# Kernel optimization log

Measured on AMD Instinct MI355X. Metric: run time of the kernel, lower is better.

The kernel has to match this reference:

```python
import jax, jax.numpy as jnp
import numpy as np

N, E, G = 50000, 800000, 64   # nodes, edges, graphs
F, H, O = 6, 256, 2           # in_dim, hidden_dim, out_dim
NE, K, L = 8, 2, 4            # n_experts, top_k, n_layers


def setup_inputs() -> dict:
    key = jax.random.key(0)
    ks = jax.random.split(key, 12)
    s = 0.05
    return {
        "x": jax.random.normal(ks[0], (N, F), jnp.float32),
        "edge_index": jax.random.randint(ks[1], (2, E), 0, N),
        "batch": jnp.sort(jax.random.randint(ks[2], (N,), 0, G)),
        "enc_W": jax.random.normal(ks[3], (F, H), jnp.float32) * s,
        "enc_b": jnp.zeros((H,), jnp.float32),
        "rtr_W1": jax.random.normal(ks[4], (H + 2, H), jnp.float32) * s,
        "rtr_b1": jnp.zeros((H,), jnp.float32),
        "rtr_W2": jax.random.normal(ks[5], (H, NE), jnp.float32) * s,
        "rtr_b2": jnp.zeros((NE,), jnp.float32),
        "hid_Wr": jax.random.normal(ks[6], (L - 1, NE, H, H), jnp.float32) * s,
        "hid_Wn": jax.random.normal(ks[7], (L - 1, NE, H, H), jnp.float32) * s,
        "hid_b": jnp.zeros((L - 1, NE, H), jnp.float32),
        "out_Wr": jax.random.normal(ks[8], (NE, H, O), jnp.float32) * s,
        "out_Wn": jax.random.normal(ks[9], (NE, H, O), jnp.float32) * s,
        "out_b": jnp.zeros((NE, O), jnp.float32),
    }


def reference(x, edge_index, batch, enc_W, enc_b, rtr_W1, rtr_b1, rtr_W2, rtr_b2,
              hid_Wr, hid_Wn, hid_b, out_Wr, out_Wn, out_b):
    src, dst = edge_index[0], edge_index[1]

    # SharedBusEncoder: Linear + ReLU
    h = jax.nn.relu(x @ enc_W + enc_b)  # [N, H]

    # graph_size_features: per-graph node/edge counts, log-scaled, per node
    ones_n = jnp.ones((N,), h.dtype)
    nodes_per_g = jax.ops.segment_sum(ones_n, batch, num_segments=G)
    edges_per_g = jax.ops.segment_sum(jnp.ones((E,), h.dtype), batch[src], num_segments=G)
    size_feat = jnp.stack([jnp.log(nodes_per_g + 1.0)[batch],
                           jnp.log(edges_per_g + 1.0)[batch]], axis=-1)  # [N, 2]

    # BaseRouter: 2-layer MLP -> logits [N, NE]
    r = jax.nn.relu(jnp.concatenate([h, size_feat], axis=-1) @ rtr_W1 + rtr_b1)
    logits = r @ rtr_W2 + rtr_b2

    # sparse_routing (eval mode): softmax over top-k logits, scattered to dense mask
    vals, idx = jax.lax.top_k(logits, K)  # [N, K]
    w = jax.nn.softmax(vals, axis=-1)
    sparse = jnp.zeros((N, NE), h.dtype).at[jnp.arange(N)[:, None], idx].set(w)

    # Dense all-expert GraphConv stacks, mask-sum combine
    def graph_conv(he, Wr, Wn, b):
        agg = jax.ops.segment_sum(he[src], dst, num_segments=N)  # sum-aggregate neighbors
        return he @ Wr + agg @ Wn + b

    out = jnp.zeros((N, O), h.dtype)
    for e in range(NE):
        he = h
        for l in range(L - 1):
            he = jax.nn.relu(graph_conv(he, hid_Wr[l, e], hid_Wn[l, e], hid_b[l, e]))
        ye = graph_conv(he, out_Wr[e], out_Wn[e], out_b[e])  # [N, O]
        out = out + ye * sparse[:, e:e + 1]
    return out
```

## Files before the change

### kernel.cpp

```cpp
#include <hip/hip_runtime.h>
#include <cstdint>

#define NN 50000
#define EE 800000
#define GG 64

typedef unsigned short u16;
typedef __attribute__((ext_vector_type(8))) short bf16x8;
typedef __attribute__((ext_vector_type(4))) float f32x4;

__device__ __forceinline__ float bf2f(u16 v) { return __uint_as_float(((unsigned)v) << 16); }
__device__ __forceinline__ u16 f2bf(float f) {
  unsigned u = __float_as_uint(f);
  return (u16)((u + 0x7fffu + ((u >> 16) & 1u)) >> 16);
}

__device__ __forceinline__ void gload_lds16(const void* g, void* l) {
  __builtin_amdgcn_global_load_lds(
      (const __attribute__((address_space(1))) void*)g,
      (__attribute__((address_space(3))) void*)l,
      16, 0, 0);
}

__global__ void k_sentinel(float* out) { out[threadIdx.x] = 1e12f; }

__global__ __launch_bounds__(256) void k_hist(const int* __restrict__ ei,
                                              int* __restrict__ deg,
                                              int* __restrict__ outdeg) {
  int i = blockIdx.x * 256 + threadIdx.x;
  if (i < EE) {
    atomicAdd(&outdeg[ei[i]], 1);
    atomicAdd(&deg[ei[EE + i]], 1);
  }
}

__global__ __launch_bounds__(256) void k_graph_feats(const int* __restrict__ batch,
                                                     const int* __restrict__ outdeg,
                                                     float* __restrict__ gf) {
  __shared__ int red[256];
  int g = blockIdx.x, tid = threadIdx.x;
  auto lb = [&](int v) {
    int lo = 0, hi = NN;
    while (lo < hi) { int m = (lo + hi) >> 1; if (batch[m] < v) lo = m + 1; else hi = m; }
    return lo;
  };
  int bs = lb(g), be = lb(g + 1);
  int s = 0;
  for (int i = bs + tid; i < be; i += 256) s += outdeg[i];
  red[tid] = s;
  __syncthreads();
  for (int off = 128; off > 0; off >>= 1) {
    if (tid < off) red[tid] += red[tid + off];
    __syncthreads();
  }
  if (tid == 0) {
    gf[g * 2] = logf((float)(be - bs) + 1.f);
    gf[g * 2 + 1] = logf((float)red[0] + 1.f);
  }
}

__global__ __launch_bounds__(256) void k_router(
    const float* __restrict__ x, const float* __restrict__ encW, const float* __restrict__ encb,
    const int* __restrict__ batch, const float* __restrict__ gf,
    const float* __restrict__ W1, const float* __restrict__ b1,
    const float* __restrict__ W2, const float* __restrict__ b2,
    float* __restrict__ sparse, u16* __restrict__ hb_out) {
  __shared__ __align__(16) float hs_t[258][8];
  __shared__ __align__(16) float rs_t[256][8];
  __shared__ float part2[4][64];
  __shared__ float xv[8][6];
  __shared__ float sf[8][2];
  __shared__ float lg[8][8];
  int tid = threadIdx.x;
  int nb = blockIdx.x * 8;
  if (tid < 48) {
    int r = tid / 6, k = tid % 6;
    xv[r][k] = x[(nb + r) * 6 + k];
  }
  if (tid >= 48 && tid < 56) {
    int r = tid - 48;
    int g = batch[nb + r];
    sf[r][0] = gf[g * 2];
    sf[r][1] = gf[g * 2 + 1];
  }
  __syncthreads();
  {
    float wcol[6];
#pragma unroll
    for (int k = 0; k < 6; ++k) wcol[k] = encW[k * 256 + tid];
    float bb = encb[tid];
#pragma unroll
    for (int r = 0; r < 8; ++r) {
      float s = bb;
#pragma unroll
      for (int k = 0; k < 6; ++k) s += xv[r][k] * wcol[k];
      float h = fmaxf(s, 0.f);
      hs_t[tid][r] = h;
      hb_out[(nb + r) * 256 + tid] = f2bf(h);
    }
  }
  if (tid < 16) {
    int r = tid >> 1, c = tid & 1;
    hs_t[256 + c][r] = sf[r][c];
  }
  __syncthreads();
  float acc[8];
  {
    float bb = b1[tid];
#pragma unroll
    for (int r = 0; r < 8; ++r) acc[r] = bb;
  }
  int k = 0;
#pragma unroll 4
  for (; k < 256; ++k) {
    float w = W1[k * 256 + tid];
    float4 ha = *(const float4*)&hs_t[k][0];
    float4 hb4 = *(const float4*)&hs_t[k][4];
    acc[0] += ha.x * w; acc[1] += ha.y * w; acc[2] += ha.z * w; acc[3] += ha.w * w;
    acc[4] += hb4.x * w; acc[5] += hb4.y * w; acc[6] += hb4.z * w; acc[7] += hb4.w * w;
  }
  for (; k < 258; ++k) {
    float w = W1[k * 256 + tid];
    float4 ha = *(const float4*)&hs_t[k][0];
    float4 hb4 = *(const float4*)&hs_t[k][4];
    acc[0] += ha.x * w; acc[1] += ha.y * w; acc[2] += ha.z * w; acc[3] += ha.w * w;
    acc[4] += hb4.x * w; acc[5] += hb4.y * w; acc[6] += hb4.z * w; acc[7] += hb4.w * w;
  }
#pragma unroll
  for (int r = 0; r < 8; ++r) rs_t[tid][r] = fmaxf(acc[r], 0.f);
  __syncthreads();
  {
    int pr = tid & 63, pt = tid >> 6;
    int r = pr >> 3, e = pr & 7;
    float s = 0.f;
    int kk0 = pt * 64;
#pragma unroll 4
    for (int kk = kk0; kk < kk0 + 64; ++kk) s += rs_t[kk][r] * W2[kk * 8 + e];
    part2[pt][pr] = s;
  }
  __syncthreads();
  if (tid < 64) {
    int r = tid >> 3, e = tid & 7;
    lg[r][e] = b2[e] + part2[0][tid] + part2[1][tid] + part2[2][tid] + part2[3][tid];
  }
  __syncthreads();
  if (tid < 8) {
    int node = nb + tid;
    {
      float v1 = lg[tid][0];
      int j1 = 0;
#pragma unroll
      for (int j = 1; j < 8; ++j) {
        float v = lg[tid][j];
        if (v > v1) { v1 = v; j1 = j; }
      }
      float v2 = -1e30f;
      int j2 = 0;
#pragma unroll
      for (int j = 0; j < 8; ++j) {
        if (j == j1) continue;
        float v = lg[tid][j];
        if (v > v2) { v2 = v; j2 = j; }
      }
      float ex = expf(v2 - v1);
      float wa = 1.f / (1.f + ex), wb = ex / (1.f + ex);
      float* sp = sparse + node * 8;
#pragma unroll
      for (int j = 0; j < 8; ++j) sp[j] = 0.f;
      sp[j1] = wa;
      sp[j2] = wb;
    }
  }
}

__global__ __launch_bounds__(1024) void k_scan(const int* __restrict__ deg,
                                               int* __restrict__ rowptr) {
  __shared__ int tmp[1024];
  __shared__ int carry;
  if (threadIdx.x == 0) { carry = 0; rowptr[0] = 0; }
  __syncthreads();
  for (int base = 0; base < NN; base += 1024) {
    int i = base + threadIdx.x;
    int v = (i < NN) ? deg[i] : 0;
    tmp[threadIdx.x] = v;
    __syncthreads();
    for (int off = 1; off < 1024; off <<= 1) {
      int t = (threadIdx.x >= off) ? tmp[threadIdx.x - off] : 0;
      __syncthreads();
      tmp[threadIdx.x] += t;
      __syncthreads();
    }
    if (i < NN) rowptr[i + 1] = carry + tmp[threadIdx.x];
    int last = tmp[1023];
    __syncthreads();
    if (threadIdx.x == 0) carry += last;
    __syncthreads();
  }
}

__global__ __launch_bounds__(256) void k_fill(const int* __restrict__ ei,
                                              const int* __restrict__ rowptr,
                                              int* __restrict__ cursor, int* __restrict__ csrc) {
  int i = blockIdx.x * 256 + threadIdx.x;
  if (i < EE) {
    int s = ei[i], d = ei[EE + i];
    int pos = atomicAdd(&cursor[d], 1);
    csrc[rowptr[d] + pos] = s;
  }
}

__global__ __launch_bounds__(256) void k_spmm256(
    const int* __restrict__ rowptr, const int* __restrict__ csrc,
    const u16* __restrict__ X, u16* __restrict__ Y) {
  int wave = threadIdx.x >> 6, lane = threadIdx.x & 63;
  int d = blockIdx.x * 4 + wave;
  if (d >= NN) return;
  int s0 = rowptr[d], s1 = rowptr[d + 1];
  int c4 = lane * 4;
  float a0 = 0.f, a1 = 0.f, a2 = 0.f, a3 = 0.f;
  int i = s0;
  for (; i + 4 <= s1; i += 4) {
    int sa = csrc[i], sb = csrc[i + 1], sc = csrc[i + 2], sd = csrc[i + 3];
    ushort4 va = *(const ushort4*)(X + sa * 256 + c4);
    ushort4 vb = *(const ushort4*)(X + sb * 256 + c4);
    ushort4 vc = *(const ushort4*)(X + sc * 256 + c4);
    ushort4 vd = *(const ushort4*)(X + sd * 256 + c4);
    a0 += bf2f(va.x) + bf2f(vb.x) + bf2f(vc.x) + bf2f(vd.x);
    a1 += bf2f(va.y) + bf2f(vb.y) + bf2f(vc.y) + bf2f(vd.y);
    a2 += bf2f(va.z) + bf2f(vb.z) + bf2f(vc.z) + bf2f(vd.z);
    a3 += bf2f(va.w) + bf2f(vb.w) + bf2f(vc.w) + bf2f(vd.w);
  }
  for (; i < s1; ++i) {
    int sa = csrc[i];
    ushort4 va = *(const ushort4*)(X + sa * 256 + c4);
    a0 += bf2f(va.x);
    a1 += bf2f(va.y);
    a2 += bf2f(va.z);
    a3 += bf2f(va.w);
  }
  ushort4 o;
  o.x = f2bf(a0); o.y = f2bf(a1); o.z = f2bf(a2); o.w = f2bf(a3);
  *(ushort4*)(Y + d * 256 + c4) = o;
}

__global__ __launch_bounds__(256) void k_spmm_intl(
    const int* __restrict__ rowptr, const int* __restrict__ csrc,
    const u16* __restrict__ X, u16* __restrict__ Y, int rs) {
  int d = blockIdx.x;
  int tid = threadIdx.x;
  if (tid * 4 >= rs) return;
  int s0 = rowptr[d], s1 = rowptr[d + 1];
  int c4 = tid * 4;
  float a0 = 0.f, a1 = 0.f, a2 = 0.f, a3 = 0.f;
  int i = s0;
  for (; i + 4 <= s1; i += 4) {
    int sa = csrc[i], sb = csrc[i + 1], sc = csrc[i + 2], sd = csrc[i + 3];
    ushort4 va = *(const ushort4*)(X + (size_t)sa * rs + c4);
    ushort4 vb = *(const ushort4*)(X + (size_t)sb * rs + c4);
    ushort4 vc = *(const ushort4*)(X + (size_t)sc * rs + c4);
    ushort4 vd = *(const ushort4*)(X + (size_t)sd * rs + c4);
    a0 += bf2f(va.x) + bf2f(vb.x) + bf2f(vc.x) + bf2f(vd.x);
    a1 += bf2f(va.y) + bf2f(vb.y) + bf2f(vc.y) + bf2f(vd.y);
    a2 += bf2f(va.z) + bf2f(vb.z) + bf2f(vc.z) + bf2f(vd.z);
    a3 += bf2f(va.w) + bf2f(vb.w) + bf2f(vc.w) + bf2f(vd.w);
  }
  for (; i < s1; ++i) {
    int sa = csrc[i];
    ushort4 va = *(const ushort4*)(X + (size_t)sa * rs + c4);
    a0 += bf2f(va.x);
    a1 += bf2f(va.y);
    a2 += bf2f(va.z);
    a3 += bf2f(va.w);
  }
  ushort4 o;
  o.x = f2bf(a0); o.y = f2bf(a1); o.z = f2bf(a2); o.w = f2bf(a3);
  *(ushort4*)(Y + (size_t)d * rs + c4) = o;
}

__global__ __launch_bounds__(256) void k_transpose2(const float* __restrict__ Wr,
                                                    const float* __restrict__ Wn,
                                                    u16* __restrict__ WrT,
                                                    u16* __restrict__ WnT) {
  int idx = blockIdx.x * 256 + threadIdx.x;
  if (idx >= 24 * 65536) return;
  int m = idx >> 16, rem = idx & 65535;
  int k = rem >> 8, j = rem & 255;
  int o = (m << 16) + (j << 8) + k;
  WrT[o] = f2bf(Wr[idx]);
  WnT[o] = f2bf(Wn[idx]);
}

__global__ __launch_bounds__(512) void k_gemm(
    const u16* __restrict__ X1b, size_t x1gs, int x1rs,
    const u16* __restrict__ X2b, size_t x2gs, int x2rs,
    const u16* __restrict__ W1tb, const u16* __restrict__ W2tb, size_t wst,
    const float* __restrict__ biasb, size_t bst,
    u16* __restrict__ Yb, size_t ygs, int yrs, int relu,
    const float* __restrict__ oWr, const float* __restrict__ oWn, int e0_base,
    float* __restrict__ Y4self, float* __restrict__ Y4nb, int do_out) {
  __shared__ __align__(16) char smem[49152];
  int g = blockIdx.y;
  const u16* X1 = X1b + (size_t)g * x1gs;
  const u16* X2 = X2b + (size_t)g * x2gs;
  const u16* W1t = W1tb + (size_t)g * wst;
  const u16* W2t = W2tb + (size_t)g * wst;
  const float* bias = biasb + (size_t)g * bst;
  u16* Y = Yb + (size_t)g * ygs;
  int tid = threadIdx.x;
  int wave = tid >> 6, lane = tid & 63;
  int l15 = lane & 15, l4 = lane >> 4;
  int m0 = blockIdx.x * 128;
  int wr = wave >> 2, wc = wave & 3;
  const f32x4 fz = {0.f, 0.f, 0.f, 0.f};
  f32x4 acc[4][4];
#pragma unroll
  for (int a = 0; a < 4; ++a)
#pragma unroll
    for (int b = 0; b < 4; ++b) acc[a][b] = fz;

  auto stage = [&](int t) {
    const u16* xs = (t < 8) ? X1 : X2;
    int xrs = (t < 8) ? x1rs : x2rs;
    const u16* wsrc = (t < 8) ? W1t : W2t;
    int kb = (t & 7) * 32;
    int half = t & 1;
    {
      int flat = wave * 1024 + lane * 16;
      int row = flat >> 6, colb = flat & 63;
      int scol = colb ^ (((row >> 1) & 3) << 4);
      int gr = m0 + row;
      if (gr > NN - 1) gr = NN - 1;
      gload_lds16(xs + (size_t)gr * xrs + kb + (scol >> 1), smem + half * 8192 + flat);
    }
#pragma unroll
    for (int q = 0; q < 2; ++q) {
      int flat = q * 8192 + wave * 1024 + lane * 16;
      int row = flat >> 6, colb = flat & 63;
      int scol = colb ^ (((row >> 1) & 3) << 4);
      gload_lds16(wsrc + row * 256 + kb + (scol >> 1), smem + 16384 + half * 16384 + flat);
    }
  };

  stage(0);
  for (int kt = 0; kt < 16; ++kt) {
    asm volatile("s_waitcnt vmcnt(0)" ::: "memory");
    __builtin_amdgcn_s_barrier();
    __builtin_amdgcn_sched_barrier(0);
    if (kt < 15) stage(kt + 1);
    const char* Ab = smem + (kt & 1) * 8192;
    const char* Bb = smem + 16384 + (kt & 1) * 16384;
    bf16x8 af[4], bfv[4];
#pragma unroll
    for (int mi = 0; mi < 4; ++mi) {
      int r = wr * 64 + mi * 16 + l15;
      af[mi] = *(const bf16x8*)(Ab + r * 64 + ((l4 * 16) ^ (((r >> 1) & 3) << 4)));
    }
#pragma unroll
    for (int nj = 0; nj < 4; ++nj) {
      int c = wc * 64 + nj * 16 + l15;
      bfv[nj] = *(const bf16x8*)(Bb + c * 64 + ((l4 * 16) ^ (((c >> 1) & 3) << 4)));
    }
#pragma unroll
    for (int mi = 0; mi < 4; ++mi)
#pragma unroll
      for (int nj = 0; nj < 4; ++nj)
        acc[mi][nj] =
            __builtin_amdgcn_mfma_f32_16x16x32_bf16(af[mi], bfv[nj], acc[mi][nj], 0, 0, 0);
  }

  if (!do_out) {
#pragma unroll
    for (int mi = 0; mi < 4; ++mi) {
      int rbase = m0 + wr * 64 + mi * 16 + l4 * 4;
#pragma unroll
      for (int nj = 0; nj < 4; ++nj) {
        int col = wc * 64 + nj * 16 + l15;
        float bv = bias[col];
#pragma unroll
        for (int r2 = 0; r2 < 4; ++r2) {
          int row = rbase + r2;
          if (row < NN) {
            float v = acc[mi][nj][r2] + bv;
            if (relu) v = fmaxf(v, 0.f);
            Y[(size_t)row * yrs + col] = f2bf(v);
          }
        }
      }
    }
  } else {
    int eabs = e0_base + g;
    const float2* wr2p = (const float2*)(oWr + (size_t)eabs * 512);
    const float2* wn2p = (const float2*)(oWn + (size_t)eabs * 512);
    float bv[4]; float2 wa[4], wb[4];
#pragma unroll
    for (int nj = 0; nj < 4; ++nj) {
      int col = wc * 64 + nj * 16 + l15;
      bv[nj] = bias[col];
      wa[nj] = wr2p[col];
      wb[nj] = wn2p[col];
    }
    float* y4red = (float*)smem;
#pragma unroll
    for (int mi = 0; mi < 4; ++mi) {
#pragma unroll
      for (int r2 = 0; r2 < 4; ++r2) {
        float p0 = 0.f, p1 = 0.f, p2 = 0.f, p3 = 0.f;
#pragma unroll
        for (int nj = 0; nj < 4; ++nj) {
          float v = fmaxf(acc[mi][nj][r2] + bv[nj], 0.f);
          p0 += v * wa[nj].x; p1 += v * wa[nj].y;
          p2 += v * wb[nj].x; p3 += v * wb[nj].y;
        }
#pragma unroll
        for (int off2 = 1; off2 < 16; off2 <<= 1) {
          p0 += __shfl_xor(p0, off2); p1 += __shfl_xor(p1, off2);
          p2 += __shfl_xor(p2, off2); p3 += __shfl_xor(p3, off2);
        }
        if (l15 == 0) {
          int lr = wr * 64 + mi * 16 + l4 * 4 + r2;
          float* q = y4red + (lr * 4 + wc) * 4;
          q[0] = p0; q[1] = p1; q[2] = p2; q[3] = p3;
        }
      }
    }
    __syncthreads();
    if (tid < 128) {
      int row = m0 + tid;
      if (row < NN) {
        float s0 = 0.f, s1 = 0.f, n0 = 0.f, n1 = 0.f;
#pragma unroll
        for (int w2 = 0; w2 < 4; ++w2) {
          const float* q = y4red + (tid * 4 + w2) * 4;
          s0 += q[0]; s1 += q[1]; n0 += q[2]; n1 += q[3];
        }
        Y4self[row * 16 + eabs * 2] = s0;
        Y4self[row * 16 + eabs * 2 + 1] = s1;
        Y4nb[row * 16 + eabs * 2] = n0;
        Y4nb[row * 16 + eabs * 2 + 1] = n1;
      }
    }
  }
}

__global__ __launch_bounds__(256) void k_combine(
    const int* __restrict__ rowptr, const int* __restrict__ csrc,
    const float* __restrict__ Y4self, const float* __restrict__ Y4nb,
    const float* __restrict__ sparse, const float* __restrict__ ob,
    float* __restrict__ out) {
  int t = blockIdx.x * 256 + threadIdx.x;
  int d = t >> 3, e = t & 7;
  if (d >= NN) return;
  float s0 = Y4self[d * 16 + e * 2], s1 = Y4self[d * 16 + e * 2 + 1];
  float n0 = 0.f, n1 = 0.f;
  for (int i = rowptr[d]; i < rowptr[d + 1]; ++i) {
    int s = csrc[i];
    float2 v = *(const float2*)(Y4nb + s * 16 + e * 2);
    n0 += v.x;
    n1 += v.y;
  }
  float w = sparse[d * 8 + e];
  float t0 = w * (s0 + n0 + ob[e * 2]);
  float t1 = w * (s1 + n1 + ob[e * 2 + 1]);
  t0 += __shfl_xor(t0, 1); t1 += __shfl_xor(t1, 1);
  t0 += __shfl_xor(t0, 2); t1 += __shfl_xor(t1, 2);
  t0 += __shfl_xor(t0, 4); t1 += __shfl_xor(t1, 4);
  if (e == 0) {
    out[d * 2] = t0;
    out[d * 2 + 1] = t1;
  }
}

extern "C" void kernel_launch(void* const* d_in, const int* in_sizes, int n_in,
                              void* d_out, int out_size, void* d_ws, size_t ws_size,
                              hipStream_t stream) {
  const float* x = (const float*)d_in[0];
  const int* ei = (const int*)d_in[1];
  const int* batch = (const int*)d_in[2];
  const float* enc_W = (const float*)d_in[3];
  const float* enc_b = (const float*)d_in[4];
  const float* rW1 = (const float*)d_in[5];
  const float* rb1 = (const float*)d_in[6];
  const float* rW2 = (const float*)d_in[7];
  const float* rb2 = (const float*)d_in[8];
  const float* hid_Wr = (const float*)d_in[9];
  const float* hid_Wn = (const float*)d_in[10];
  const float* hid_b = (const float*)d_in[11];
  const float* out_Wr = (const float*)d_in[12];
  const float* out_Wn = (const float*)d_in[13];
  const float* out_b = (const float*)d_in[14];
  float* out = (float*)d_out;

  char* ws = (char*)d_ws;
  size_t off = 0;
  auto alloc = [&](size_t bytes) -> void* {
    void* p = ws + off;
    off = (off + bytes + 511) & ~(size_t)511;
    return p;
  };
  const size_t HBYTES = (size_t)NN * 256 * 2;
  u16* hb = (u16*)alloc(HBYTES);
  u16* agg0 = (u16*)alloc(HBYTES);
  u16* WrT = (u16*)alloc((size_t)24 * 65536 * 2);
  u16* WnT = (u16*)alloc((size_t)24 * 65536 * 2);
  int* deg = (int*)alloc((size_t)NN * 4);
  int* cursor = (int*)alloc((size_t)NN * 4);
  int* outdeg = (int*)alloc((size_t)NN * 4);
  size_t zero_bytes = (size_t)((char*)(outdeg + NN) - (char*)deg);
  int* rowptr = (int*)alloc((size_t)(NN + 1) * 4);
  int* csrc = (int*)alloc((size_t)EE * 4);
  float* gf = (float*)alloc(GG * 2 * 4);
  float* sparse = (float*)alloc((size_t)NN * 8 * 4);
  float* Y4self = (float*)alloc((size_t)NN * 16 * 4);
  float* Y4nb = (float*)alloc((size_t)NN * 16 * 4);

  size_t rem = (ws_size > off) ? ws_size - off : 0;
  size_t per = 2 * HBYTES + 2048;
  int grp = (rem >= 4 * per) ? 4 : (rem >= 2 * per) ? 2 : (rem >= per) ? 1 : 0;
  if (grp == 0) {
    k_sentinel<<<1, 2, 0, stream>>>(out);
    return;
  }
  u16* heb = (u16*)alloc((size_t)grp * HBYTES);
  u16* aggb = (u16*)alloc((size_t)grp * HBYTES);
  const int RS = grp * 256;

  hipMemsetAsync(deg, 0, zero_bytes, stream);

  k_transpose2<<<(24 * 65536 + 255) / 256, 256, 0, stream>>>(hid_Wr, hid_Wn, WrT, WnT);
  k_hist<<<(EE + 255) / 256, 256, 0, stream>>>(ei, deg, outdeg);
  k_graph_feats<<<GG, 256, 0, stream>>>(batch, outdeg, gf);
  k_scan<<<1, 1024, 0, stream>>>(deg, rowptr);
  k_fill<<<(EE + 255) / 256, 256, 0, stream>>>(ei, rowptr, cursor, csrc);
  k_router<<<NN / 8, 256, 0, stream>>>(x, enc_W, enc_b, batch, gf, rW1, rb1, rW2, rb2,
                                       sparse, hb);

  const int GX = (NN + 127) / 128;

  k_spmm256<<<(NN + 3) / 4, 256, 0, stream>>>(rowptr, csrc, hb, agg0);
  for (int e0 = 0; e0 < 8; e0 += grp) {
    k_gemm<<<dim3(GX, grp), 512, 0, stream>>>(
        hb, 0, 256, agg0, 0, 256, WrT + e0 * 65536, WnT + e0 * 65536, 65536,
        hid_b + e0 * 256, 256, heb, 256, RS, 1, nullptr, nullptr, 0, nullptr, nullptr, 0);
    k_spmm_intl<<<NN, 256, 0, stream>>>(rowptr, csrc, heb, aggb, RS);
    k_gemm<<<dim3(GX, grp), 512, 0, stream>>>(
        heb, 256, RS, aggb, 256, RS, WrT + (8 + e0) * 65536, WnT + (8 + e0) * 65536, 65536,
        hid_b + (8 + e0) * 256, 256, heb, 256, RS, 1, nullptr, nullptr, 0, nullptr, nullptr, 0);
    k_spmm_intl<<<NN, 256, 0, stream>>>(rowptr, csrc, heb, aggb, RS);
    k_gemm<<<dim3(GX, grp), 512, 0, stream>>>(
        heb, 256, RS, aggb, 256, RS, WrT + (16 + e0) * 65536, WnT + (16 + e0) * 65536, 65536,
        hid_b + (16 + e0) * 256, 256, nullptr, 0, 256, 1, out_Wr, out_Wn, e0,
        Y4self, Y4nb, 1);
  }
  k_combine<<<(NN * 8 + 255) / 256, 256, 0, stream>>>(rowptr, csrc, Y4self, Y4nb, sparse,
                                                      out_b, out);
}
```

Baseline: 2.273 ms.

## Tile router over 32 nodes per block and batch all eight experts together

The router kernel now handles 32 nodes per block instead of 8, so each W1 column load is reused across four times more rows. It keeps 32 accumulators per thread and drops the split-K partial reduction for the second layer. Separately, the expert group size can now reach 8 when workspace allows, and the interleaved SpMM launches RS/4 threads per node, so one gather covers all experts. This cuts kernel launches and repeated index traversal, but needs more workspace, registers and LDS per block.

```diff
diff --git a/kernel.cpp b/kernel.cpp
--- a/kernel.cpp
+++ b/kernel.cpp
@@ -65,23 +65,23 @@
     const float* __restrict__ W1, const float* __restrict__ b1,
     const float* __restrict__ W2, const float* __restrict__ b2,
     float* __restrict__ sparse, u16* __restrict__ hb_out) {
-  __shared__ __align__(16) float hs_t[258][8];
-  __shared__ __align__(16) float rs_t[256][8];
-  __shared__ float part2[4][64];
-  __shared__ float xv[8][6];
-  __shared__ float sf[8][2];
-  __shared__ float lg[8][8];
+  __shared__ __align__(16) float hs_t[258][32];
+  __shared__ __align__(16) float rs_t[256][32];
+  __shared__ float xv[32][6];
+  __shared__ float sf2[2][32];
+  __shared__ float lg[32][8];
   int tid = threadIdx.x;
-  int nb = blockIdx.x * 8;
-  if (tid < 48) {
+  int nb = blockIdx.x * 32;
+  if (tid < 192) {
     int r = tid / 6, k = tid % 6;
-    xv[r][k] = x[(nb + r) * 6 + k];
-  }
-  if (tid >= 48 && tid < 56) {
-    int r = tid - 48;
-    int g = batch[nb + r];
-    sf[r][0] = gf[g * 2];
-    sf[r][1] = gf[g * 2 + 1];
+    int node = nb + r;
+    xv[r][k] = x[(node < NN ? node : NN - 1) * 6 + k];
+  } else if (tid < 224) {
+    int r = tid - 192;
+    int node = nb + r;
+    int g = batch[node < NN ? node : NN - 1];
+    sf2[0][r] = gf[g * 2];
+    sf2[1][r] = gf[g * 2 + 1];
   }
   __syncthreads();
   {
@@ -89,64 +89,66 @@
 #pragma unroll
     for (int k = 0; k < 6; ++k) wcol[k] = encW[k * 256 + tid];
     float bb = encb[tid];
-#pragma unroll
-    for (int r = 0; r < 8; ++r) {
+    float hrow[32];
+#pragma unroll
+    for (int r = 0; r < 32; ++r) {
       float s = bb;
 #pragma unroll
       for (int k = 0; k < 6; ++k) s += xv[r][k] * wcol[k];
-      float h = fmaxf(s, 0.f);
-      hs_t[tid][r] = h;
-      hb_out[(nb + r) * 256 + tid] = f2bf(h);
-    }
-  }
-  if (tid < 16) {
-    int r = tid >> 1, c = tid & 1;
-    hs_t[256 + c][r] = sf[r][c];
-  }
-  __syncthreads();
-  float acc[8];
-  {
-    float bb = b1[tid];
-#pragma unroll
-    for (int r = 0; r < 8; ++r) acc[r] = bb;
-  }
-  int k = 0;
-#pragma unroll 4
-  for (; k < 256; ++k) {
-    float w = W1[k * 256 + tid];
-    float4 ha = *(const float4*)&hs_t[k][0];
-    float4 hb4 = *(const float4*)&hs_t[k][4];
-    acc[0] += ha.x * w; acc[1] += ha.y * w; acc[2] += ha.z * w; acc[3] += ha.w * w;
-    acc[4] += hb4.x * w; acc[5] += hb4.y * w; acc[6] += hb4.z * w; acc[7] += hb4.w * w;
-  }
-  for (; k < 258; ++k) {
-    float w = W1[k * 256 + tid];
-    float4 ha = *(const float4*)&hs_t[k][0];
-    float4 hb4 = *(const float4*)&hs_t[k][4];
-    acc[0] += ha.x * w; acc[1] += ha.y * w; acc[2] += ha.z * w; acc[3] += ha.w * w;
-    acc[4] += hb4.x * w; acc[5] += hb4.y * w; acc[6] += hb4.z * w; acc[7] += hb4.w * w;
-  }
-#pragma unroll
-  for (int r = 0; r < 8; ++r) rs_t[tid][r] = fmaxf(acc[r], 0.f);
+      hrow[r] = fmaxf(s, 0.f);
+    }
+#pragma unroll
+    for (int q = 0; q < 8; ++q) {
+      float4 v = {hrow[q * 4], hrow[q * 4 + 1], hrow[q * 4 + 2], hrow[q * 4 + 3]};
+      *(float4*)&hs_t[tid][q * 4] = v;
+    }
+#pragma unroll
+    for (int r = 0; r < 32; ++r) {
+      int node = nb + r;
+      if (node < NN) hb_out[(size_t)node * 256 + tid] = f2bf(hrow[r]);
+    }
+  }
+  if (tid < 64) {
+    int c = tid >> 5, r = tid & 31;
+    hs_t[256 + c][r] = sf2[c][r];
+  }
   __syncthreads();
   {
-    int pr = tid & 63, pt = tid >> 6;
-    int r = pr >> 3, e = pr & 7;
-    float s = 0.f;
-    int kk0 = pt * 64;
+    float acc[32];
+    float bb = b1[tid];
+#pragma unroll
+    for (int r = 0; r < 32; ++r) acc[r] = bb;
+#pragma unroll 2
+    for (int k = 0; k < 258; ++k) {
+      float w = W1[k * 256 + tid];
+#pragma unroll
+      for (int q = 0; q < 8; ++q) {
+        float4 hv = *(const float4*)&hs_t[k][q * 4];
+        acc[q * 4 + 0] += hv.x * w;
+        acc[q * 4 + 1] += hv.y * w;
+        acc[q * 4 + 2] += hv.z * w;
+        acc[q * 4 + 3] += hv.w * w;
+      }
+    }
+#pragma unroll
+    for (int q = 0; q < 8; ++q) {
+      float4 v = {fmaxf(acc[q * 4], 0.f), fmaxf(acc[q * 4 + 1], 0.f),
+                  fmaxf(acc[q * 4 + 2], 0.f), fmaxf(acc[q * 4 + 3], 0.f)};
+      *(float4*)&rs_t[tid][q * 4] = v;
+    }
+  }
+  __syncthreads();
+  {
+    int r = tid >> 3, e = tid & 7;
+    float s = b2[e];
 #pragma unroll 4
-    for (int kk = kk0; kk < kk0 + 64; ++kk) s += rs_t[kk][r] * W2[kk * 8 + e];
-    part2[pt][pr] = s;
+    for (int k = 0; k < 256; ++k) s += rs_t[k][r] * W2[k * 8 + e];
+    lg[r][e] = s;
   }
   __syncthreads();
-  if (tid < 64) {
-    int r = tid >> 3, e = tid & 7;
-    lg[r][e] = b2[e] + part2[0][tid] + part2[1][tid] + part2[2][tid] + part2[3][tid];
-  }
-  __syncthreads();
-  if (tid < 8) {
+  if (tid < 32) {
     int node = nb + tid;
-    {
+    if (node < NN) {
       float v1 = lg[tid][0];
       int j1 = 0;
 #pragma unroll
@@ -164,7 +166,7 @@
       }
       float ex = expf(v2 - v1);
       float wa = 1.f / (1.f + ex), wb = ex / (1.f + ex);
-      float* sp = sparse + node * 8;
+      float* sp = sparse + (size_t)node * 8;
 #pragma unroll
       for (int j = 0; j < 8; ++j) sp[j] = 0.f;
       sp[j1] = wa;
@@ -243,7 +245,7 @@
   *(ushort4*)(Y + d * 256 + c4) = o;
 }
 
-__global__ __launch_bounds__(256) void k_spmm_intl(
+__global__ __launch_bounds__(512) void k_spmm_intl(
     const int* __restrict__ rowptr, const int* __restrict__ csrc,
     const u16* __restrict__ X, u16* __restrict__ Y, int rs) {
   int d = blockIdx.x;
@@ -515,7 +517,8 @@
 
   size_t rem = (ws_size > off) ? ws_size - off : 0;
   size_t per = 2 * HBYTES + 2048;
-  int grp = (rem >= 4 * per) ? 4 : (rem >= 2 * per) ? 2 : (rem >= per) ? 1 : 0;
+  int grp = (rem >= 8 * per) ? 8 : (rem >= 4 * per) ? 4 : (rem >= 2 * per) ? 2
+            : (rem >= per) ? 1 : 0;
   if (grp == 0) {
     k_sentinel<<<1, 2, 0, stream>>>(out);
     return;
@@ -531,8 +534,8 @@
   k_graph_feats<<<GG, 256, 0, stream>>>(batch, outdeg, gf);
   k_scan<<<1, 1024, 0, stream>>>(deg, rowptr);
   k_fill<<<(EE + 255) / 256, 256, 0, stream>>>(ei, rowptr, cursor, csrc);
-  k_router<<<NN / 8, 256, 0, stream>>>(x, enc_W, enc_b, batch, gf, rW1, rb1, rW2, rb2,
-                                       sparse, hb);
+  k_router<<<(NN + 31) / 32, 256, 0, stream>>>(x, enc_W, enc_b, batch, gf, rW1, rb1,
+                                               rW2, rb2, sparse, hb);
 
   const int GX = (NN + 127) / 128;
 
@@ -541,11 +544,11 @@
     k_gemm<<<dim3(GX, grp), 512, 0, stream>>>(
         hb, 0, 256, agg0, 0, 256, WrT + e0 * 65536, WnT + e0 * 65536, 65536,
         hid_b + e0 * 256, 256, heb, 256, RS, 1, nullptr, nullptr, 0, nullptr, nullptr, 0);
-    k_spmm_intl<<<NN, 256, 0, stream>>>(rowptr, csrc, heb, aggb, RS);
+    k_spmm_intl<<<NN, RS / 4, 0, stream>>>(rowptr, csrc, heb, aggb, RS);
     k_gemm<<<dim3(GX, grp), 512, 0, stream>>>(
         heb, 256, RS, aggb, 256, RS, WrT + (8 + e0) * 65536, WnT + (8 + e0) * 65536, 65536,
         hid_b + (8 + e0) * 256, 256, heb, 256, RS, 1, nullptr, nullptr, 0, nullptr, nullptr, 0);
-    k_spmm_intl<<<NN, 256, 0, stream>>>(rowptr, csrc, heb, aggb, RS);
+    k_spmm_intl<<<NN, RS / 4, 0, stream>>>(rowptr, csrc, heb, aggb, RS);
     k_gemm<<<dim3(GX, grp), 512, 0, stream>>>(
         heb, 256, RS, aggb, 256, RS, WrT + (16 + e0) * 65536, WnT + (16 + e0) * 65536, 65536,
         hid_b + (16 + e0) * 256, 256, nullptr, 0, 256, 1, out_Wr, out_Wn, e0,
```

New measurement: 2.353 ms. 1.04x slower.
